# Kernel optimization log

Measured on AMD Instinct MI355X. Metric: run time of the kernel, lower is better.

## Reference

```python
import jax, jax.numpy as jnp
import numpy as np

N = 50000      # nodes
E = 625000     # edges
D = 128        # in/hidden channels (equal, required by skip connection)
L = 64         # latent dim
NLAYER = 3
EPS = 1e-5     # batchnorm eps
SLOPE = 0.01   # leaky_relu default negative slope


def setup_inputs() -> dict:
    key = jax.random.key(0)
    ks = jax.random.split(key, 8)
    s = 1.0 / np.sqrt(D)
    x = jax.random.normal(ks[0], (N, D), dtype=jnp.float32)
    edge_index = jax.random.randint(ks[1], (2, E), 0, N, dtype=jnp.int64)
    Ws = jax.random.normal(ks[2], (NLAYER, D, D), dtype=jnp.float32) * s
    bs = jnp.zeros((NLAYER, D), dtype=jnp.float32)
    Wmu = jax.random.normal(ks[3], (D, L), dtype=jnp.float32) * s
    bmu = jnp.zeros((L,), dtype=jnp.float32)
    Wlv = jax.random.normal(ks[4], (D, L), dtype=jnp.float32) * s
    blv = jnp.zeros((L,), dtype=jnp.float32)
    gamma = jnp.ones((D,), dtype=jnp.float32)
    beta = jnp.zeros((D,), dtype=jnp.float32)
    return dict(x=x, edge_index=edge_index, Ws=Ws, bs=bs, Wmu=Wmu, bmu=bmu,
                Wlv=Wlv, blv=blv, gamma=gamma, beta=beta)


def reference(x, edge_index, Ws, bs, Wmu, bmu, Wlv, blv, gamma, beta):
    n = x.shape[0]
    self_idx = jnp.arange(n, dtype=edge_index.dtype)
    src = jnp.concatenate([edge_index[0], self_idx])  # [E+N] with self-loops
    dst = jnp.concatenate([edge_index[1], self_idx])
    # symmetric GCN normalization: deg counted on destination (incl. self-loops)
    deg = jax.ops.segment_sum(jnp.ones(src.shape[0], dtype=x.dtype), dst, num_segments=n)
    dinv = jax.lax.rsqrt(jnp.maximum(deg, 1e-12))  # deg >= 1 thanks to self-loops
    norm = dinv[src] * dinv[dst]                   # [E+N]

    def gcn(h, W, b):
        h = h @ W                                  # transform then propagate (PyG GCNConv)
        msg = h[src] * norm[:, None]               # gather + per-edge scale
        return jax.ops.segment_sum(msg, dst, num_segments=n) + b

    for i in range(NLAYER):
        x_res = x
        x = gcn(x, Ws[i], bs[i])
        # BatchNorm (training mode: batch statistics, biased variance)
        mean = jnp.mean(x, axis=0)
        var = jnp.var(x, axis=0)
        x = (x - mean) * jax.lax.rsqrt(var + EPS) * gamma + beta
        x = jnp.where(x >= 0, x, SLOPE * x)        # leaky_relu
        x = x + x_res                              # skip connection

    mu = gcn(x, Wmu, bmu)
    logvar = gcn(x, Wlv, blv)
    return (mu, logvar)
```

## Files before the change

### kernel.cpp

```cpp
#include <hip/hip_runtime.h>

typedef unsigned int uint;
typedef unsigned short ushort;

#define EPS 1e-5f
#define SLOPE 0.01f
#define GATHER_BLOCKS 2048
#define PK 136

static inline int cdiv(long a, int b) { return (int)((a + b - 1) / b); }

typedef __attribute__((ext_vector_type(8))) short short8;
typedef __attribute__((ext_vector_type(4))) float f32x4;

__device__ inline float bf_lo(uint v) { return __uint_as_float(v << 16); }
__device__ inline float bf_hi(uint v) { return __uint_as_float(v & 0xffff0000u); }
__device__ inline ushort f2bf(float f) {
  uint u = __float_as_uint(f);
  u += 0x7fffu + ((u >> 16) & 1u);
  return (ushort)(u >> 16);
}
__device__ inline uint pack2bf(float a, float b) {
  return (uint)f2bf(a) | ((uint)f2bf(b) << 16);
}

__global__ void deg_kernel(const int* __restrict__ dst, int* __restrict__ degi, int E) {
  int e = blockIdx.x * 256 + threadIdx.x;
  if (e < E) atomicAdd(&degi[dst[e]], 1);
}

__global__ __launch_bounds__(256) void bsum_kernel(const int* __restrict__ degi,
    int* __restrict__ bsum, float* __restrict__ dinv, int n) {
  int tid = threadIdx.x;
  int i = blockIdx.x * 256 + tid;
  int v = (i < n) ? degi[i] : 0;
  if (i < n) dinv[i] = rsqrtf((float)(v + 1));
  int r = (v + 3) & ~3;
  #pragma unroll
  for (int ofs = 32; ofs; ofs >>= 1) r += __shfl_down(r, ofs, 64);
  __shared__ int ws[4];
  if ((tid & 63) == 0) ws[tid >> 6] = r;
  __syncthreads();
  if (tid == 0) bsum[blockIdx.x] = ws[0] + ws[1] + ws[2] + ws[3];
}

__global__ __launch_bounds__(256) void bscan_kernel(const int* __restrict__ bsum,
    int* __restrict__ bofs, int* __restrict__ ptr_end, int nb) {
  int tid = threadIdx.x, lane = tid & 63, wv = tid >> 6;
  __shared__ int wsum[4];
  __shared__ int carry_s, tot_s;
  if (tid == 0) carry_s = 0;
  __syncthreads();
  for (int base = 0; base < nb; base += 256) {
    int i = base + tid;
    int v = (i < nb) ? bsum[i] : 0;
    int inc = v;
    #pragma unroll
    for (int ofs = 1; ofs < 64; ofs <<= 1) {
      int t = __shfl_up(inc, ofs, 64);
      if (lane >= ofs) inc += t;
    }
    if (lane == 63) wsum[wv] = inc;
    __syncthreads();
    if (tid == 0) {
      int a = carry_s;
      for (int w = 0; w < 4; ++w) { int t = wsum[w]; wsum[w] = a; a += t; }
      tot_s = a;
    }
    __syncthreads();
    if (i < nb) bofs[i] = wsum[wv] + inc - v;
    __syncthreads();
    if (tid == 0) carry_s = tot_s;
    __syncthreads();
  }
  if (tid == 0) *ptr_end = carry_s;
}

__global__ __launch_bounds__(256) void ptr_kernel(const int* __restrict__ degi,
    const int* __restrict__ bofs, int* __restrict__ ptr, int n) {
  int tid = threadIdx.x, lane = tid & 63, wv = tid >> 6;
  int i = blockIdx.x * 256 + tid;
  int v = (i < n) ? ((degi[i] + 3) & ~3) : 0;
  int inc = v;
  #pragma unroll
  for (int ofs = 1; ofs < 64; ofs <<= 1) {
    int t = __shfl_up(inc, ofs, 64);
    if (lane >= ofs) inc += t;
  }
  __shared__ int wsum[4], woff[4];
  if (lane == 63) wsum[wv] = inc;
  __syncthreads();
  if (tid == 0) {
    int a = 0;
    for (int w = 0; w < 4; ++w) { woff[w] = a; a += wsum[w]; }
  }
  __syncthreads();
  if (i < n) ptr[i] = bofs[blockIdx.x] + woff[wv] + inc - v;
}

__global__ void fill_kernel(const int* __restrict__ src, const int* __restrict__ dst,
    const float* __restrict__ dinv, const int* __restrict__ ptr,
    int* __restrict__ fillc, uint* __restrict__ csr, int E) {
  int e = blockIdx.x * 256 + threadIdx.x;
  if (e >= E) return;
  int s = src[e], d = dst[e];
  int pos = ptr[d] + atomicAdd(&fillc[d], 1);
  float c = dinv[s] * dinv[d];
  csr[pos] = (uint)s | ((uint)f2bf(c) << 16);
}

template<bool FUSED, bool WRITEX, bool TWOW, bool XRESBF>
__global__ __launch_bounds__(256) void mfma_gemm(
    const float* __restrict__ Af, const uint* __restrict__ Az,
    const float* __restrict__ scale, const float* __restrict__ shift,
    const float* __restrict__ xresf, const uint* __restrict__ xresb,
    uint* __restrict__ xoutb,
    const float* __restrict__ W0, const float* __restrict__ W1,
    ushort* __restrict__ Cbf, int n) {
  __shared__ ushort sWt[128 * PK];
  const int tid = threadIdx.x;
  for (int t = tid; t < 1024; t += 256) {
    const int tk = t & 31;
    const int tc = t >> 5;
    float4 r0, r1, r2, r3;
    if (TWOW) {
      int c = tc * 4;
      const float* Wb = (c < 64) ? W0 : W1;
      int cc = (c < 64) ? c : c - 64;
      r0 = *(const float4*)&Wb[(tk * 4 + 0) * 64 + cc];
      r1 = *(const float4*)&Wb[(tk * 4 + 1) * 64 + cc];
      r2 = *(const float4*)&Wb[(tk * 4 + 2) * 64 + cc];
      r3 = *(const float4*)&Wb[(tk * 4 + 3) * 64 + cc];
    } else {
      r0 = *(const float4*)&W0[(tk * 4 + 0) * 128 + tc * 4];
      r1 = *(const float4*)&W0[(tk * 4 + 1) * 128 + tc * 4];
      r2 = *(const float4*)&W0[(tk * 4 + 2) * 128 + tc * 4];
      r3 = *(const float4*)&W0[(tk * 4 + 3) * 128 + tc * 4];
    }
    const float* p0 = (const float*)&r0;
    const float* p1 = (const float*)&r1;
    const float* p2 = (const float*)&r2;
    const float* p3 = (const float*)&r3;
    #pragma unroll
    for (int j = 0; j < 4; ++j) {
      uint lo = (uint)f2bf(p0[j]) | ((uint)f2bf(p1[j]) << 16);
      uint hi = (uint)f2bf(p2[j]) | ((uint)f2bf(p3[j]) << 16);
      *(uint2*)&sWt[(tc * 4 + j) * PK + tk * 4] = make_uint2(lo, hi);
    }
  }
  __syncthreads();

  const int w = tid >> 6;
  const int lane = tid & 63;
  const int l16 = lane & 15, q = lane >> 4;
  const int row0 = blockIdx.x * 128 + w * 32;

  f32x4 acc[2][8];
  #pragma unroll
  for (int mt = 0; mt < 2; ++mt)
    #pragma unroll
    for (int nt = 0; nt < 8; ++nt)
      acc[mt][nt] = (f32x4){0.f, 0.f, 0.f, 0.f};

  for (int ks = 0; ks < 4; ++ks) {
    const int kbase = ks * 32 + q * 8;
    short8 afrag[2];
    #pragma unroll
    for (int mt = 0; mt < 2; ++mt) {
      int row = row0 + mt * 16 + l16;
      float av[8] = {0.f,0.f,0.f,0.f,0.f,0.f,0.f,0.f};
      if (row < n) {
        if constexpr (FUSED) {
          uint4 zw = *(const uint4*)&Az[(size_t)row * 64 + (kbase >> 1)];
          float zv[8] = { bf_lo(zw.x), bf_hi(zw.x), bf_lo(zw.y), bf_hi(zw.y),
                          bf_lo(zw.z), bf_hi(zw.z), bf_lo(zw.w), bf_hi(zw.w) };
          float4 sc0 = *(const float4*)&scale[kbase];
          float4 sc1 = *(const float4*)&scale[kbase + 4];
          float4 sh0 = *(const float4*)&shift[kbase];
          float4 sh1 = *(const float4*)&shift[kbase + 4];
          float scv[8] = { sc0.x, sc0.y, sc0.z, sc0.w, sc1.x, sc1.y, sc1.z, sc1.w };
          float shv[8] = { sh0.x, sh0.y, sh0.z, sh0.w, sh1.x, sh1.y, sh1.z, sh1.w };
          float xv[8];
          if constexpr (XRESBF) {
            uint4 xw = *(const uint4*)&xresb[(size_t)row * 64 + (kbase >> 1)];
            xv[0]=bf_lo(xw.x); xv[1]=bf_hi(xw.x); xv[2]=bf_lo(xw.y); xv[3]=bf_hi(xw.y);
            xv[4]=bf_lo(xw.z); xv[5]=bf_hi(xw.z); xv[6]=bf_lo(xw.w); xv[7]=bf_hi(xw.w);
          } else {
            const float* Xr = xresf + (size_t)row * 128 + kbase;
            float4 x0 = *(const float4*)&Xr[0];
            float4 x1 = *(const float4*)&Xr[4];
            xv[0]=x0.x; xv[1]=x0.y; xv[2]=x0.z; xv[3]=x0.w;
            xv[4]=x1.x; xv[5]=x1.y; xv[6]=x1.z; xv[7]=x1.w;
          }
          #pragma unroll
          for (int j = 0; j < 8; ++j) {
            float u = fmaf(zv[j], scv[j], shv[j]);
            u = u >= 0.f ? u : SLOPE * u;
            av[j] = u + xv[j];
          }
          if constexpr (WRITEX) {
            uint4 o;
            o.x = pack2bf(av[0], av[1]); o.y = pack2bf(av[2], av[3]);
            o.z = pack2bf(av[4], av[5]); o.w = pack2bf(av[6], av[7]);
            *(uint4*)&xoutb[(size_t)row * 64 + (kbase >> 1)] = o;
          }
        } else {
          const float* Ar = Af + (size_t)row * 128 + kbase;
          float4 a0 = *(const float4*)&Ar[0];
          float4 a1 = *(const float4*)&Ar[4];
          av[0]=a0.x; av[1]=a0.y; av[2]=a0.z; av[3]=a0.w;
          av[4]=a1.x; av[5]=a1.y; av[6]=a1.z; av[7]=a1.w;
        }
      }
      short8 af;
      #pragma unroll
      for (int j = 0; j < 8; ++j) af[j] = (short)f2bf(av[j]);
      afrag[mt] = af;
    }
    #pragma unroll
    for (int nt = 0; nt < 8; ++nt) {
      short8 bfrag = *(const short8*)&sWt[(nt * 16 + l16) * PK + kbase];
      acc[0][nt] = __builtin_amdgcn_mfma_f32_16x16x32_bf16(afrag[0], bfrag, acc[0][nt], 0, 0, 0);
      acc[1][nt] = __builtin_amdgcn_mfma_f32_16x16x32_bf16(afrag[1], bfrag, acc[1][nt], 0, 0, 0);
    }
  }
  #pragma unroll
  for (int mt = 0; mt < 2; ++mt) {
    int rbase = row0 + mt * 16 + q * 4;
    #pragma unroll
    for (int nt = 0; nt < 8; ++nt) {
      int col = nt * 16 + l16;
      #pragma unroll
      for (int r = 0; r < 4; ++r) {
        int row = rbase + r;
        if (row < n) Cbf[(size_t)row * 128 + col] = f2bf(acc[mt][nt][r]);
      }
    }
  }
}

#define EDGE_FMA(E_, R_, AX_, AY_) { float c_ = bf_hi(E_); \
  AX_ = fmaf(c_, bf_lo(R_), AX_); AY_ = fmaf(c_, bf_hi(R_), AY_); }

__global__ __launch_bounds__(256) void gather_layer(const int* __restrict__ ptr,
    const uint* __restrict__ csr, const uint* __restrict__ ybf,
    const float* __restrict__ b, const float* __restrict__ dinv,
    uint* __restrict__ zbf, float* __restrict__ psum, float* __restrict__ psq, int n) {
  const int tid = threadIdx.x;
  const int lane = tid & 63, wv = tid >> 6;
  float2 bb = *(const float2*)&b[lane * 2];
  float sx = 0.f, sy = 0.f, qx = 0.f, qy = 0.f;
  const int wstride = gridDim.x * 4;
  for (int w = blockIdx.x * 4 + wv; w < n; w += wstride) {
    float dv = dinv[w], c0 = dv * dv;
    uint yv = ybf[(size_t)w * 64 + lane];
    float ax = fmaf(c0, bf_lo(yv), bb.x);
    float ay = fmaf(c0, bf_hi(yv), bb.y);
    int j = ptr[w], end = ptr[w + 1];
    while (j + 8 <= end) {
      uint4 ea = *(const uint4*)&csr[j];
      uint4 eb = *(const uint4*)&csr[j + 4];
      uint r0 = ybf[(size_t)(ea.x & 0xffffu) * 64 + lane];
      uint r1 = ybf[(size_t)(ea.y & 0xffffu) * 64 + lane];
      uint r2 = ybf[(size_t)(ea.z & 0xffffu) * 64 + lane];
      uint r3 = ybf[(size_t)(ea.w & 0xffffu) * 64 + lane];
      uint r4 = ybf[(size_t)(eb.x & 0xffffu) * 64 + lane];
      uint r5 = ybf[(size_t)(eb.y & 0xffffu) * 64 + lane];
      uint r6 = ybf[(size_t)(eb.z & 0xffffu) * 64 + lane];
      uint r7 = ybf[(size_t)(eb.w & 0xffffu) * 64 + lane];
      EDGE_FMA(ea.x, r0, ax, ay); EDGE_FMA(ea.y, r1, ax, ay);
      EDGE_FMA(ea.z, r2, ax, ay); EDGE_FMA(ea.w, r3, ax, ay);
      EDGE_FMA(eb.x, r4, ax, ay); EDGE_FMA(eb.y, r5, ax, ay);
      EDGE_FMA(eb.z, r6, ax, ay); EDGE_FMA(eb.w, r7, ax, ay);
      j += 8;
    }
    if (j < end) {
      uint4 ea = *(const uint4*)&csr[j];
      uint r0 = ybf[(size_t)(ea.x & 0xffffu) * 64 + lane];
      uint r1 = ybf[(size_t)(ea.y & 0xffffu) * 64 + lane];
      uint r2 = ybf[(size_t)(ea.z & 0xffffu) * 64 + lane];
      uint r3 = ybf[(size_t)(ea.w & 0xffffu) * 64 + lane];
      EDGE_FMA(ea.x, r0, ax, ay); EDGE_FMA(ea.y, r1, ax, ay);
      EDGE_FMA(ea.z, r2, ax, ay); EDGE_FMA(ea.w, r3, ax, ay);
    }
    zbf[(size_t)w * 64 + lane] = pack2bf(ax, ay);
    sx += ax; sy += ay;
    qx = fmaf(ax, ax, qx); qy = fmaf(ay, ay, qy);
  }
  __shared__ float red[4][64];
  red[wv][lane] = sx; __syncthreads();
  if (wv == 0) psum[(size_t)blockIdx.x * 128 + lane * 2] =
      red[0][lane] + red[1][lane] + red[2][lane] + red[3][lane];
  __syncthreads();
  red[wv][lane] = sy; __syncthreads();
  if (wv == 0) psum[(size_t)blockIdx.x * 128 + lane * 2 + 1] =
      red[0][lane] + red[1][lane] + red[2][lane] + red[3][lane];
  __syncthreads();
  red[wv][lane] = qx; __syncthreads();
  if (wv == 0) psq[(size_t)blockIdx.x * 128 + lane * 2] =
      red[0][lane] + red[1][lane] + red[2][lane] + red[3][lane];
  __syncthreads();
  red[wv][lane] = qy; __syncthreads();
  if (wv == 0) psq[(size_t)blockIdx.x * 128 + lane * 2 + 1] =
      red[0][lane] + red[1][lane] + red[2][lane] + red[3][lane];
}

__global__ __launch_bounds__(256) void gather_heads(const int* __restrict__ ptr,
    const uint* __restrict__ csr, const uint* __restrict__ ybf,
    const float* __restrict__ bmu, const float* __restrict__ blv,
    const float* __restrict__ dinv, float* __restrict__ out, int n) {
  const int tid = threadIdx.x;
  const int lane = tid & 63, wv = tid >> 6;
  int col = lane * 2;
  const float* bias; size_t obase; int cc;
  if (col < 64) { obase = 0; bias = bmu; cc = col; }
  else { obase = (size_t)n * 64; bias = blv; cc = col - 64; }
  float bx = bias[cc], by = bias[cc + 1];
  const int wstride = gridDim.x * 4;
  for (int w = blockIdx.x * 4 + wv; w < n; w += wstride) {
    float dv = dinv[w], c0 = dv * dv;
    uint yv = ybf[(size_t)w * 64 + lane];
    float ax = fmaf(c0, bf_lo(yv), bx);
    float ay = fmaf(c0, bf_hi(yv), by);
    int j = ptr[w], end = ptr[w + 1];
    while (j + 8 <= end) {
      uint4 ea = *(const uint4*)&csr[j];
      uint4 eb = *(const uint4*)&csr[j + 4];
      uint r0 = ybf[(size_t)(ea.x & 0xffffu) * 64 + lane];
      uint r1 = ybf[(size_t)(ea.y & 0xffffu) * 64 + lane];
      uint r2 = ybf[(size_t)(ea.z & 0xffffu) * 64 + lane];
      uint r3 = ybf[(size_t)(ea.w & 0xffffu) * 64 + lane];
      uint r4 = ybf[(size_t)(eb.x & 0xffffu) * 64 + lane];
      uint r5 = ybf[(size_t)(eb.y & 0xffffu) * 64 + lane];
      uint r6 = ybf[(size_t)(eb.z & 0xffffu) * 64 + lane];
      uint r7 = ybf[(size_t)(eb.w & 0xffffu) * 64 + lane];
      EDGE_FMA(ea.x, r0, ax, ay); EDGE_FMA(ea.y, r1, ax, ay);
      EDGE_FMA(ea.z, r2, ax, ay); EDGE_FMA(ea.w, r3, ax, ay);
      EDGE_FMA(eb.x, r4, ax, ay); EDGE_FMA(eb.y, r5, ax, ay);
      EDGE_FMA(eb.z, r6, ax, ay); EDGE_FMA(eb.w, r7, ax, ay);
      j += 8;
    }
    if (j < end) {
      uint4 ea = *(const uint4*)&csr[j];
      uint r0 = ybf[(size_t)(ea.x & 0xffffu) * 64 + lane];
      uint r1 = ybf[(size_t)(ea.y & 0xffffu) * 64 + lane];
      uint r2 = ybf[(size_t)(ea.z & 0xffffu) * 64 + lane];
      uint r3 = ybf[(size_t)(ea.w & 0xffffu) * 64 + lane];
      EDGE_FMA(ea.x, r0, ax, ay); EDGE_FMA(ea.y, r1, ax, ay);
      EDGE_FMA(ea.z, r2, ax, ay); EDGE_FMA(ea.w, r3, ax, ay);
    }
    *(float2*)&out[obase + (size_t)w * 64 + cc] = make_float2(ax, ay);
  }
}

__global__ __launch_bounds__(256) void bnfin_kernel(const float* __restrict__ psum,
    const float* __restrict__ psq, const float* __restrict__ gamma,
    const float* __restrict__ beta, float* __restrict__ scale,
    float* __restrict__ shift, int n, int nb) {
  const int c = blockIdx.x;
  const int tid = threadIdx.x;
  float s = 0.f, s2 = 0.f;
  for (int b = tid; b < nb; b += 256) {
    s += psum[(size_t)b * 128 + c];
    s2 += psq[(size_t)b * 128 + c];
  }
  #pragma unroll
  for (int ofs = 32; ofs; ofs >>= 1) {
    s += __shfl_down(s, ofs, 64);
    s2 += __shfl_down(s2, ofs, 64);
  }
  __shared__ float ws[4], wq[4];
  if ((tid & 63) == 0) { ws[tid >> 6] = s; wq[tid >> 6] = s2; }
  __syncthreads();
  if (tid == 0) {
    float S = ws[0] + ws[1] + ws[2] + ws[3];
    float Q = wq[0] + wq[1] + wq[2] + wq[3];
    float mean = S / (float)n;
    float var = Q / (float)n - mean * mean;
    float inv = rsqrtf(var + EPS);
    float sc = gamma[c] * inv;
    scale[c] = sc;
    shift[c] = beta[c] - mean * sc;
  }
}

extern "C" void kernel_launch(void* const* d_in, const int* in_sizes, int n_in,
                              void* d_out, int out_size, void* d_ws, size_t ws_size,
                              hipStream_t stream) {
  const float* x     = (const float*)d_in[0];
  const int*   ei    = (const int*)d_in[1];
  const float* Ws    = (const float*)d_in[2];
  const float* bs    = (const float*)d_in[3];
  const float* Wmu   = (const float*)d_in[4];
  const float* bmu   = (const float*)d_in[5];
  const float* Wlv   = (const float*)d_in[6];
  const float* blv   = (const float*)d_in[7];
  const float* gamma = (const float*)d_in[8];
  const float* beta  = (const float*)d_in[9];
  float* out = (float*)d_out;

  const int n = in_sizes[0] / 128;
  const int E = in_sizes[1] / 2;
  const int* srcI = ei;
  const int* dstI = ei + E;
  const int nb = cdiv(n, 256);
  const size_t Epad = (size_t)E + 3 * (size_t)n;

  char* wsp = (char*)d_ws;
  size_t off = 0;
  auto alloc = [&](size_t bytes) -> void* {
    void* p = wsp + off;
    off += (bytes + 255) & ~(size_t)255;
    return p;
  };
  int*    degi  = (int*)alloc(((size_t)2 * n + Epad) * 4);
  int*    fillc = degi + n;
  uint*   csr   = (uint*)(degi + 2 * n);
  float*  dinv  = (float*)alloc((size_t)n * 4);
  int*    ptr   = (int*)alloc((size_t)(n + 1) * 4);
  int*    bsum  = (int*)alloc((size_t)nb * 4);
  int*    bofs  = (int*)alloc((size_t)nb * 4);
  ushort* ybf   = (ushort*)alloc((size_t)n * 128 * 2);
  uint*   zbf   = (uint*)alloc((size_t)n * 64 * 4);
  uint*   xbbf  = (uint*)alloc((size_t)n * 64 * 4);
  float*  psum  = (float*)alloc((size_t)GATHER_BLOCKS * 128 * 4);
  float*  psq   = (float*)alloc((size_t)GATHER_BLOCKS * 128 * 4);
  float*  scale = (float*)alloc(128 * 4);
  float*  shift = (float*)alloc(128 * 4);
  (void)n_in; (void)out_size; (void)ws_size;

  hipMemsetAsync(degi, 0, ((size_t)2 * n + Epad) * 4, stream);
  deg_kernel<<<cdiv(E, 256), 256, 0, stream>>>(dstI, degi, E);
  bsum_kernel<<<nb, 256, 0, stream>>>(degi, bsum, dinv, n);
  bscan_kernel<<<1, 256, 0, stream>>>(bsum, bofs, ptr + n, nb);
  ptr_kernel<<<nb, 256, 0, stream>>>(degi, bofs, ptr, n);
  fill_kernel<<<cdiv(E, 256), 256, 0, stream>>>(srcI, dstI, dinv, ptr, fillc, csr, E);

  const int ggrid = cdiv(n, 128);

  mfma_gemm<false, false, false, false><<<ggrid, 256, 0, stream>>>(
      x, nullptr, nullptr, nullptr, nullptr, nullptr, nullptr, Ws, nullptr, ybf, n);
  gather_layer<<<GATHER_BLOCKS, 256, 0, stream>>>(ptr, csr, (const uint*)ybf, bs, dinv, zbf, psum, psq, n);
  bnfin_kernel<<<128, 256, 0, stream>>>(psum, psq, gamma, beta, scale, shift, n, GATHER_BLOCKS);
  mfma_gemm<true, true, false, false><<<ggrid, 256, 0, stream>>>(
      nullptr, zbf, scale, shift, x, nullptr, xbbf, Ws + 16384, nullptr, ybf, n);
  gather_layer<<<GATHER_BLOCKS, 256, 0, stream>>>(ptr, csr, (const uint*)ybf, bs + 128, dinv, zbf, psum, psq, n);
  bnfin_kernel<<<128, 256, 0, stream>>>(psum, psq, gamma, beta, scale, shift, n, GATHER_BLOCKS);
  mfma_gemm<true, true, false, true><<<ggrid, 256, 0, stream>>>(
      nullptr, zbf, scale, shift, nullptr, xbbf, xbbf, Ws + 32768, nullptr, ybf, n);
  gather_layer<<<GATHER_BLOCKS, 256, 0, stream>>>(ptr, csr, (const uint*)ybf, bs + 256, dinv, zbf, psum, psq, n);
  bnfin_kernel<<<128, 256, 0, stream>>>(psum, psq, gamma, beta, scale, shift, n, GATHER_BLOCKS);
  mfma_gemm<true, false, true, true><<<ggrid, 256, 0, stream>>>(
      nullptr, zbf, scale, shift, nullptr, xbbf, nullptr, Wmu, Wlv, ybf, n);
  gather_heads<<<GATHER_BLOCKS, 256, 0, stream>>>(ptr, csr, (const uint*)ybf, bmu, blv, dinv, out, n);
}
```

Baseline: 263.5 us.

## Split features into column quarters so gather working set fits cache

```diff
diff --git a/kernel.cpp b/kernel.cpp
--- a/kernel.cpp
+++ b/kernel.cpp
@@ -154,6 +154,8 @@
   const int lane = tid & 63;
   const int l16 = lane & 15, q = lane >> 4;
   const int row0 = blockIdx.x * 128 + w * 32;
+  const size_t n16 = (size_t)n * 16;
+  const size_t n32 = (size_t)n * 32;
 
   f32x4 acc[2][8];
   #pragma unroll
@@ -171,7 +173,7 @@
       float av[8] = {0.f,0.f,0.f,0.f,0.f,0.f,0.f,0.f};
       if (row < n) {
         if constexpr (FUSED) {
-          uint4 zw = *(const uint4*)&Az[(size_t)row * 64 + (kbase >> 1)];
+          uint4 zw = *(const uint4*)&Az[(size_t)ks * n16 + (size_t)row * 16 + q * 4];
           float zv[8] = { bf_lo(zw.x), bf_hi(zw.x), bf_lo(zw.y), bf_hi(zw.y),
                           bf_lo(zw.z), bf_hi(zw.z), bf_lo(zw.w), bf_hi(zw.w) };
           float4 sc0 = *(const float4*)&scale[kbase];
@@ -230,10 +232,12 @@
     #pragma unroll
     for (int nt = 0; nt < 8; ++nt) {
       int col = nt * 16 + l16;
+      ushort* yq = Cbf + (size_t)(col >> 5) * n32;
+      int cw = col & 31;
       #pragma unroll
       for (int r = 0; r < 4; ++r) {
         int row = rbase + r;
-        if (row < n) Cbf[(size_t)row * 128 + col] = f2bf(acc[mt][nt][r]);
+        if (row < n) yq[(size_t)row * 32 + cw] = f2bf(acc[mt][nt][r]);
       }
     }
   }
@@ -243,113 +247,116 @@
   AX_ = fmaf(c_, bf_lo(R_), AX_); AY_ = fmaf(c_, bf_hi(R_), AY_); }
 
 __global__ __launch_bounds__(256) void gather_layer(const int* __restrict__ ptr,
-    const uint* __restrict__ csr, const uint* __restrict__ ybf,
+    const uint* __restrict__ csr, const uint* __restrict__ yq_all,
     const float* __restrict__ b, const float* __restrict__ dinv,
-    uint* __restrict__ zbf, float* __restrict__ psum, float* __restrict__ psq, int n) {
+    uint* __restrict__ zq_all, float* __restrict__ psum, float* __restrict__ psq, int n) {
   const int tid = threadIdx.x;
   const int lane = tid & 63, wv = tid >> 6;
-  float2 bb = *(const float2*)&b[lane * 2];
+  const int qd = blockIdx.x & 3;
+  const int l16 = lane & 15, g = lane >> 4;
+  const size_t n16 = (size_t)n * 16;
+  const uint* yq = yq_all + (size_t)qd * n16;
+  uint* zq = zq_all + (size_t)qd * n16;
+  const int cbase = qd * 32 + l16 * 2;
+  float2 bb = *(const float2*)&b[cbase];
   float sx = 0.f, sy = 0.f, qx = 0.f, qy = 0.f;
-  const int wstride = gridDim.x * 4;
-  for (int w = blockIdx.x * 4 + wv; w < n; w += wstride) {
-    float dv = dinv[w], c0 = dv * dv;
-    uint yv = ybf[(size_t)w * 64 + lane];
-    float ax = fmaf(c0, bf_lo(yv), bb.x);
-    float ay = fmaf(c0, bf_hi(yv), bb.y);
-    int j = ptr[w], end = ptr[w + 1];
-    while (j + 8 <= end) {
-      uint4 ea = *(const uint4*)&csr[j];
-      uint4 eb = *(const uint4*)&csr[j + 4];
-      uint r0 = ybf[(size_t)(ea.x & 0xffffu) * 64 + lane];
-      uint r1 = ybf[(size_t)(ea.y & 0xffffu) * 64 + lane];
-      uint r2 = ybf[(size_t)(ea.z & 0xffffu) * 64 + lane];
-      uint r3 = ybf[(size_t)(ea.w & 0xffffu) * 64 + lane];
-      uint r4 = ybf[(size_t)(eb.x & 0xffffu) * 64 + lane];
-      uint r5 = ybf[(size_t)(eb.y & 0xffffu) * 64 + lane];
-      uint r6 = ybf[(size_t)(eb.z & 0xffffu) * 64 + lane];
-      uint r7 = ybf[(size_t)(eb.w & 0xffffu) * 64 + lane];
-      EDGE_FMA(ea.x, r0, ax, ay); EDGE_FMA(ea.y, r1, ax, ay);
-      EDGE_FMA(ea.z, r2, ax, ay); EDGE_FMA(ea.w, r3, ax, ay);
-      EDGE_FMA(eb.x, r4, ax, ay); EDGE_FMA(eb.y, r5, ax, ay);
-      EDGE_FMA(eb.z, r6, ax, ay); EDGE_FMA(eb.w, r7, ax, ay);
-      j += 8;
+  const int wstride = (gridDim.x >> 2) * 4;
+  for (int w = (blockIdx.x >> 2) * 4 + wv; w < n; w += wstride) {
+    int beg = ptr[w], end = ptr[w + 1];
+    float ax, ay;
+    if (g == 0) {
+      float dv = dinv[w], c0 = dv * dv;
+      uint yv = yq[(size_t)w * 16 + l16];
+      ax = fmaf(c0, bf_lo(yv), bb.x);
+      ay = fmaf(c0, bf_hi(yv), bb.y);
+    } else { ax = 0.f; ay = 0.f; }
+    int j = beg + g;
+    for (; j + 4 < end; j += 8) {
+      uint e0 = __builtin_nontemporal_load(&csr[j]);
+      uint e1 = __builtin_nontemporal_load(&csr[j + 4]);
+      uint v0 = yq[(size_t)(e0 & 0xffffu) * 16 + l16];
+      uint v1 = yq[(size_t)(e1 & 0xffffu) * 16 + l16];
+      EDGE_FMA(e0, v0, ax, ay);
+      EDGE_FMA(e1, v1, ax, ay);
     }
     if (j < end) {
-      uint4 ea = *(const uint4*)&csr[j];
-      uint r0 = ybf[(size_t)(ea.x & 0xffffu) * 64 + lane];
-      uint r1 = ybf[(size_t)(ea.y & 0xffffu) * 64 + lane];
-      uint r2 = ybf[(size_t)(ea.z & 0xffffu) * 64 + lane];
-      uint r3 = ybf[(size_t)(ea.w & 0xffffu) * 64 + lane];
-      EDGE_FMA(ea.x, r0, ax, ay); EDGE_FMA(ea.y, r1, ax, ay);
-      EDGE_FMA(ea.z, r2, ax, ay); EDGE_FMA(ea.w, r3, ax, ay);
-    }
-    zbf[(size_t)w * 64 + lane] = pack2bf(ax, ay);
-    sx += ax; sy += ay;
-    qx = fmaf(ax, ax, qx); qy = fmaf(ay, ay, qy);
-  }
-  __shared__ float red[4][64];
-  red[wv][lane] = sx; __syncthreads();
-  if (wv == 0) psum[(size_t)blockIdx.x * 128 + lane * 2] =
-      red[0][lane] + red[1][lane] + red[2][lane] + red[3][lane];
-  __syncthreads();
-  red[wv][lane] = sy; __syncthreads();
-  if (wv == 0) psum[(size_t)blockIdx.x * 128 + lane * 2 + 1] =
-      red[0][lane] + red[1][lane] + red[2][lane] + red[3][lane];
-  __syncthreads();
-  red[wv][lane] = qx; __syncthreads();
-  if (wv == 0) psq[(size_t)blockIdx.x * 128 + lane * 2] =
-      red[0][lane] + red[1][lane] + red[2][lane] + red[3][lane];
-  __syncthreads();
-  red[wv][lane] = qy; __syncthreads();
-  if (wv == 0) psq[(size_t)blockIdx.x * 128 + lane * 2 + 1] =
-      red[0][lane] + red[1][lane] + red[2][lane] + red[3][lane];
+      uint e0 = __builtin_nontemporal_load(&csr[j]);
+      uint v0 = yq[(size_t)(e0 & 0xffffu) * 16 + l16];
+      EDGE_FMA(e0, v0, ax, ay);
+    }
+    ax += __shfl_xor(ax, 16, 64); ay += __shfl_xor(ay, 16, 64);
+    ax += __shfl_xor(ax, 32, 64); ay += __shfl_xor(ay, 32, 64);
+    if (g == 0) {
+      __builtin_nontemporal_store(pack2bf(ax, ay), &zq[(size_t)w * 16 + l16]);
+      sx += ax; sy += ay;
+      qx = fmaf(ax, ax, qx); qy = fmaf(ay, ay, qy);
+    }
+  }
+  __shared__ float red[4][16];
+  if (g == 0) red[wv][l16] = sx;
+  __syncthreads();
+  if (wv == 0 && g == 0) psum[(size_t)blockIdx.x * 32 + l16 * 2] =
+      red[0][l16] + red[1][l16] + red[2][l16] + red[3][l16];
+  __syncthreads();
+  if (g == 0) red[wv][l16] = sy;
+  __syncthreads();
+  if (wv == 0 && g == 0) psum[(size_t)blockIdx.x * 32 + l16 * 2 + 1] =
+      red[0][l16] + red[1][l16] + red[2][l16] + red[3][l16];
+  __syncthreads();
+  if (g == 0) red[wv][l16] = qx;
+  __syncthreads();
+  if (wv == 0 && g == 0) psq[(size_t)blockIdx.x * 32 + l16 * 2] =
+      red[0][l16] + red[1][l16] + red[2][l16] + red[3][l16];
+  __syncthreads();
+  if (g == 0) red[wv][l16] = qy;
+  __syncthreads();
+  if (wv == 0 && g == 0) psq[(size_t)blockIdx.x * 32 + l16 * 2 + 1] =
+      red[0][l16] + red[1][l16] + red[2][l16] + red[3][l16];
 }
 
 __global__ __launch_bounds__(256) void gather_heads(const int* __restrict__ ptr,
-    const uint* __restrict__ csr, const uint* __restrict__ ybf,
+    const uint* __restrict__ csr, const uint* __restrict__ yq_all,
     const float* __restrict__ bmu, const float* __restrict__ blv,
     const float* __restrict__ dinv, float* __restrict__ out, int n) {
   const int tid = threadIdx.x;
   const int lane = tid & 63, wv = tid >> 6;
-  int col = lane * 2;
-  const float* bias; size_t obase; int cc;
-  if (col < 64) { obase = 0; bias = bmu; cc = col; }
-  else { obase = (size_t)n * 64; bias = blv; cc = col - 64; }
+  const int qd = blockIdx.x & 3;
+  const int l16 = lane & 15, g = lane >> 4;
+  const size_t n16 = (size_t)n * 16;
+  const uint* yq = yq_all + (size_t)qd * n16;
+  const int cb = qd * 32 + l16 * 2;
+  const int head = cb >> 6, cc = cb & 63;
+  float* ob = out + (size_t)head * n * 64;
+  const float* bias = head ? blv : bmu;
   float bx = bias[cc], by = bias[cc + 1];
-  const int wstride = gridDim.x * 4;
-  for (int w = blockIdx.x * 4 + wv; w < n; w += wstride) {
-    float dv = dinv[w], c0 = dv * dv;
-    uint yv = ybf[(size_t)w * 64 + lane];
-    float ax = fmaf(c0, bf_lo(yv), bx);
-    float ay = fmaf(c0, bf_hi(yv), by);
-    int j = ptr[w], end = ptr[w + 1];
-    while (j + 8 <= end) {
-      uint4 ea = *(const uint4*)&csr[j];
-      uint4 eb = *(const uint4*)&csr[j + 4];
-      uint r0 = ybf[(size_t)(ea.x & 0xffffu) * 64 + lane];
-      uint r1 = ybf[(size_t)(ea.y & 0xffffu) * 64 + lane];
-      uint r2 = ybf[(size_t)(ea.z & 0xffffu) * 64 + lane];
-      uint r3 = ybf[(size_t)(ea.w & 0xffffu) * 64 + lane];
-      uint r4 = ybf[(size_t)(eb.x & 0xffffu) * 64 + lane];
-      uint r5 = ybf[(size_t)(eb.y & 0xffffu) * 64 + lane];
-      uint r6 = ybf[(size_t)(eb.z & 0xffffu) * 64 + lane];
-      uint r7 = ybf[(size_t)(eb.w & 0xffffu) * 64 + lane];
-      EDGE_FMA(ea.x, r0, ax, ay); EDGE_FMA(ea.y, r1, ax, ay);
-      EDGE_FMA(ea.z, r2, ax, ay); EDGE_FMA(ea.w, r3, ax, ay);
-      EDGE_FMA(eb.x, r4, ax, ay); EDGE_FMA(eb.y, r5, ax, ay);
-      EDGE_FMA(eb.z, r6, ax, ay); EDGE_FMA(eb.w, r7, ax, ay);
-      j += 8;
+  const int wstride = (gridDim.x >> 2) * 4;
+  for (int w = (blockIdx.x >> 2) * 4 + wv; w < n; w += wstride) {
+    int beg = ptr[w], end = ptr[w + 1];
+    float ax, ay;
+    if (g == 0) {
+      float dv = dinv[w], c0 = dv * dv;
+      uint yv = yq[(size_t)w * 16 + l16];
+      ax = fmaf(c0, bf_lo(yv), bx);
+      ay = fmaf(c0, bf_hi(yv), by);
+    } else { ax = 0.f; ay = 0.f; }
+    int j = beg + g;
+    for (; j + 4 < end; j += 8) {
+      uint e0 = __builtin_nontemporal_load(&csr[j]);
+      uint e1 = __builtin_nontemporal_load(&csr[j + 4]);
+      uint v0 = yq[(size_t)(e0 & 0xffffu) * 16 + l16];
+      uint v1 = yq[(size_t)(e1 & 0xffffu) * 16 + l16];
+      EDGE_FMA(e0, v0, ax, ay);
+      EDGE_FMA(e1, v1, ax, ay);
     }
     if (j < end) {
-      uint4 ea = *(const uint4*)&csr[j];
-      uint r0 = ybf[(size_t)(ea.x & 0xffffu) * 64 + lane];
-      uint r1 = ybf[(size_t)(ea.y & 0xffffu) * 64 + lane];
-      uint r2 = ybf[(size_t)(ea.z & 0xffffu) * 64 + lane];
-      uint r3 = ybf[(size_t)(ea.w & 0xffffu) * 64 + lane];
-      EDGE_FMA(ea.x, r0, ax, ay); EDGE_FMA(ea.y, r1, ax, ay);
-      EDGE_FMA(ea.z, r2, ax, ay); EDGE_FMA(ea.w, r3, ax, ay);
-    }
-    *(float2*)&out[obase + (size_t)w * 64 + cc] = make_float2(ax, ay);
+      uint e0 = __builtin_nontemporal_load(&csr[j]);
+      uint v0 = yq[(size_t)(e0 & 0xffffu) * 16 + l16];
+      EDGE_FMA(e0, v0, ax, ay);
+    }
+    ax += __shfl_xor(ax, 16, 64); ay += __shfl_xor(ay, 16, 64);
+    ax += __shfl_xor(ax, 32, 64); ay += __shfl_xor(ay, 32, 64);
+    if (g == 0)
+      *(float2*)&ob[(size_t)w * 64 + cc] = make_float2(ax, ay);
   }
 }
 
@@ -359,10 +366,13 @@
     float* __restrict__ shift, int n, int nb) {
   const int c = blockIdx.x;
   const int tid = threadIdx.x;
+  const int qd = c >> 5, cw = c & 31;
+  const int nq = nb >> 2;
   float s = 0.f, s2 = 0.f;
-  for (int b = tid; b < nb; b += 256) {
-    s += psum[(size_t)b * 128 + c];
-    s2 += psq[(size_t)b * 128 + c];
+  for (int k = tid; k < nq; k += 256) {
+    int bidx = qd + 4 * k;
+    s += psum[(size_t)bidx * 32 + cw];
+    s2 += psq[(size_t)bidx * 32 + cw];
   }
   #pragma unroll
   for (int ofs = 32; ofs; ofs >>= 1) {
@@ -423,8 +433,8 @@
   ushort* ybf   = (ushort*)alloc((size_t)n * 128 * 2);
   uint*   zbf   = (uint*)alloc((size_t)n * 64 * 4);
   uint*   xbbf  = (uint*)alloc((size_t)n * 64 * 4);
-  float*  psum  = (float*)alloc((size_t)GATHER_BLOCKS * 128 * 4);
-  float*  psq   = (float*)alloc((size_t)GATHER_BLOCKS * 128 * 4);
+  float*  psum  = (float*)alloc((size_t)GATHER_BLOCKS * 32 * 4);
+  float*  psq   = (float*)alloc((size_t)GATHER_BLOCKS * 32 * 4);
   float*  scale = (float*)alloc(128 * 4);
   float*  shift = (float*)alloc(128 * 4);
   (void)n_in; (void)out_size; (void)ws_size;
```

After: 412.0 us. 1.56x slower.
